# Kernel optimization log

Hardware: AMD Instinct MI355X
Metric: run time of the kernel (lower is better)

Reference implementation:

```python
import jax, jax.numpy as jnp
import numpy as np

B, N, C, H, D, K = 8, 2000, 64, 64, 16, 2  # batch, nodes, hidden, hidden_hidden, embed_dim, cheb_k


def setup_inputs() -> dict:
    key = jax.random.key(0)
    ks = jax.random.split(key, 12)
    f = lambda k, s, sc=1.0: jax.random.normal(k, s, dtype=jnp.float32) * sc
    return {
        "z": f(ks[0], (B, N, C)),
        "W_in": f(ks[1], (H, C), 0.1),
        "b_in": f(ks[2], (H,), 0.1),
        "W_out": f(ks[3], (C * C, H), 0.05),
        "b_out": f(ks[4], (C * C,), 0.05),
        "emb": f(ks[5], (N, D), 0.1),
        "wp": f(ks[6], (D, K, H, H), 0.1),
        "bp": f(ks[7], (D, H), 0.1),
        "w1": f(ks[8], (C,)),
        "w2": f(ks[9], (C,)),
        "vs": f(ks[10], (N, N), 0.02),
        "bs": f(ks[11], (N, N), 0.02),
    }


def reference(z, W_in, b_in, W_out, b_out, emb, wp, bp, w1, w2, vs, bs):
    # linear_in + relu: (B,N,C) -> (B,N,H)
    h = jax.nn.relu(jnp.einsum("bnc,hc->bnh", z, W_in) + b_in)

    # data-adaptive graph: softmax over rows of relu(emb @ emb^T)
    A = jax.nn.softmax(jax.nn.relu(emb @ emb.T), axis=1)  # (N,N)
    S = jnp.stack([jnp.eye(N, dtype=z.dtype), A], axis=0)  # (K,N,N), cheb_k=2

    # spatial attention on h (x = h.unsqueeze(1), f_in == H == C)
    e1 = h @ w1  # (B,N)
    e2 = h @ w2  # (B,N)
    prod = e1[:, :, None] * e2[:, None, :]  # (B,N,N) outer product
    E = jax.nn.softmax(
        jnp.einsum("nm,bmp->bnp", vs, jax.nn.sigmoid(prod + bs)), axis=-1
    )  # (B,N,N)

    # batched supports: E.unsqueeze(1) @ S -> (B,K,N,N)
    sup = jnp.einsum("bnm,kmp->bknp", E, S)

    # node-adaptive weights / bias
    weights = jnp.einsum("nd,dkio->nkio", emb, wp)  # (N,K,H,H)
    bias = emb @ bp  # (N,H)

    # graph conv
    x_g = jnp.einsum("bknm,bmc->bnkc", sup, h)  # (B,N,K,H)
    g = jnp.einsum("bnki,nkio->bno", x_g, weights) + bias  # (B,N,H)

    # linear_out + view + tanh, scaled by 0.1
    out = jnp.tanh(jnp.einsum("bnh,oh->bno", g, W_out) + b_out)
    return 0.1 * out.reshape(B, N, C, C)
```

## Files before the change

kernel.cpp:

```cpp
#include <hip/hip_runtime.h>
#include <hip/hip_bf16.h>

#define NN 2000
#define NP 2048
#define BB 8
#define HH 64
#define DD 16

typedef __hip_bfloat16 bf16;
typedef short bf16x8 __attribute__((ext_vector_type(8)));
typedef float f32x4 __attribute__((ext_vector_type(4)));

__device__ __forceinline__ float fast_sigmoid(float x) {
    return 1.0f / (1.0f + __expf(-x));
}
__device__ __forceinline__ float fast_tanh(float x) {
    float e = __expf(2.0f * x);
    return 1.0f - 2.0f / (e + 1.0f);
}

__device__ __forceinline__ void glds16(const void* g, void* l) {
    __builtin_amdgcn_global_load_lds(
        (const __attribute__((address_space(1))) void*)g,
        (__attribute__((address_space(3))) void*)l, 16, 0, 0);
}

__global__ __launch_bounds__(256) void k_h(
        const float* __restrict__ z, const float* __restrict__ W_in,
        const float* __restrict__ b_in, const float* __restrict__ w1,
        const float* __restrict__ w2, float* __restrict__ h,
        float* __restrict__ e1, float* __restrict__ e2) {
    __shared__ float WT[64 * 65];
    __shared__ float zs[4][64];
    int t = threadIdx.x;
    int lane = t & 63, ty = t >> 6;
    int bn0 = blockIdx.x * 4;
    for (int i = t; i < 64 * 64; i += 256) {
        int hh = i >> 6, c = i & 63;
        WT[c * 65 + hh] = W_in[i];
    }
    zs[ty][lane] = z[(size_t)(bn0 + ty) * 64 + lane];
    __syncthreads();
    float acc = b_in[lane];
    #pragma unroll
    for (int c = 0; c < 64; c++) acc += zs[ty][c] * WT[c * 65 + lane];
    float hv = fmaxf(acc, 0.0f);
    h[(size_t)(bn0 + ty) * 64 + lane] = hv;
    float p1 = hv * w1[lane], p2 = hv * w2[lane];
    #pragma unroll
    for (int off = 32; off > 0; off >>= 1) {
        p1 += __shfl_down(p1, off);
        p2 += __shfl_down(p2, off);
    }
    if (lane == 0) { e1[bn0 + ty] = p1; e2[bn0 + ty] = p2; }
}

__global__ __launch_bounds__(256) void k_A(const float* __restrict__ emb,
                                           bf16* __restrict__ A) {
    int i = blockIdx.x, t = threadIdx.x;
    if (i >= NN) {
        for (int j = t; j < NP; j += 256) A[(size_t)i * NP + j] = __float2bfloat16(0.0f);
        return;
    }
    __shared__ float ei[DD];
    __shared__ float rowbuf[NP];
    __shared__ float red[256];
    if (t < DD) ei[t] = emb[i * DD + t];
    __syncthreads();
    float lmax = -1e30f;
    for (int j = t; j < NP; j += 256) {
        float s = 0.0f;
        if (j < NN) {
            #pragma unroll
            for (int d = 0; d < DD; d++) s += ei[d] * emb[j * DD + d];
            s = fmaxf(s, 0.0f);
            lmax = fmaxf(lmax, s);
        }
        rowbuf[j] = s;
    }
    red[t] = lmax; __syncthreads();
    for (int o = 128; o > 0; o >>= 1) { if (t < o) red[t] = fmaxf(red[t], red[t + o]); __syncthreads(); }
    float mx = red[0];
    __syncthreads();
    float lsum = 0.0f;
    for (int j = t; j < NN; j += 256) {
        float e = __expf(rowbuf[j] - mx);
        rowbuf[j] = e; lsum += e;
    }
    red[t] = lsum; __syncthreads();
    for (int o = 128; o > 0; o >>= 1) { if (t < o) red[t] += red[t + o]; __syncthreads(); }
    float inv = 1.0f / red[0];
    for (int j = t; j < NP; j += 256)
        A[(size_t)i * NP + j] = __float2bfloat16(j < NN ? rowbuf[j] * inv : 0.0f);
}

__global__ __launch_bounds__(256) void k_misc(
        const float* __restrict__ vs, bf16* __restrict__ vs_bf,
        const float* __restrict__ W_out, bf16* __restrict__ Wo_bf,
        const float* __restrict__ emb, const float* __restrict__ wp,
        float* __restrict__ Wn_all) {
    __shared__ float embs[128 * 16];
    int bid = blockIdx.x, t = threadIdx.x;
    if (bid < 16384) {
        int id = bid * 256 + t;
        int n = id >> 11, m = id & (NP - 1);
        float v = (n < NN && m < NN) ? vs[n * NN + m] : 0.0f;
        vs_bf[id] = __float2bfloat16(v);
        return;
    }
    if (bid < 16384 + 1024) {
        int id = (bid - 16384) * 256 + t;
        Wo_bf[id] = __float2bfloat16(W_out[id]);
        return;
    }
    int wb = bid - 17408;
    int n0 = (wb & 15) * 128;
    int jo = (wb >> 4) * 256 + t;
    float wv[16];
    #pragma unroll
    for (int d = 0; d < 16; d++) wv[d] = wp[(size_t)d * 8192 + jo];
    for (int s = t; s < 128 * 16; s += 256) {
        int i = s >> 4, d = s & 15;
        int n = n0 + i;
        embs[s] = (n < NN) ? emb[n * 16 + d] : 0.f;
    }
    __syncthreads();
    for (int i = 0; i < 128; i++) {
        int n = n0 + i;
        if (n >= NN) break;
        const f32x4* ev = (const f32x4*)&embs[i * 16];
        f32x4 e0 = ev[0], e1 = ev[1], e2 = ev[2], e3 = ev[3];
        float a = 0.f;
        #pragma unroll
        for (int q = 0; q < 4; q++) a += e0[q] * wv[q];
        #pragma unroll
        for (int q = 0; q < 4; q++) a += e1[q] * wv[4 + q];
        #pragma unroll
        for (int q = 0; q < 4; q++) a += e2[q] * wv[8 + q];
        #pragma unroll
        for (int q = 0; q < 4; q++) a += e3[q] * wv[12 + q];
        Wn_all[(size_t)n * 8192 + jo] = a;
    }
}

__global__ __launch_bounds__(256) void k_hT(const float* __restrict__ h,
                                            bf16* __restrict__ hTcat,
                                            bf16* __restrict__ hsT) {
    __shared__ float tile[64 * 65];
    int nt = blockIdx.x, b = blockIdx.y;
    int tx = threadIdx.x & 63, ty = threadIdx.x >> 6;
    int n0 = nt * 64;
    for (int i = ty * 16; i < ty * 16 + 16; i++) {
        int n = n0 + i;
        tile[i * 65 + tx] = (n < NN) ? h[((size_t)b * NN + n) * 64 + tx] : 0.0f;
    }
    __syncthreads();
    for (int i = ty * 16; i < ty * 16 + 16; i++) {
        bf16 v = __float2bfloat16(tile[tx * 65 + i]);
        hTcat[((size_t)b * 64 + i) * NP + n0 + tx] = v;
        hsT[((size_t)b * 128 + i) * NP + n0 + tx] = v;
    }
}

__global__ __launch_bounds__(256) void k_redT(const float* __restrict__ AhPart,
                                              bf16* __restrict__ hsT) {
    __shared__ float tile[64 * 65];
    int pt = blockIdx.x, b = blockIdx.y;
    int tx = threadIdx.x & 63, ty = threadIdx.x >> 6;
    int p0 = pt * 64, q0 = b * 64;
    const long long TOT = (long long)NP * 512;
    for (int i = ty * 16; i < ty * 16 + 16; i++) {
        long long base = ((long long)p0 + i) * 512 + q0 + tx;
        float s = AhPart[base];
        #pragma unroll
        for (int sl = 1; sl < 4; sl++) s += AhPart[sl * TOT + base];
        tile[i * 65 + tx] = s;
    }
    __syncthreads();
    for (int i = ty * 16; i < ty * 16 + 16; i++)
        hsT[((size_t)b * 128 + 64 + i) * NP + p0 + tx] =
            __float2bfloat16(tile[tx * 65 + i]);
}

__global__ __launch_bounds__(256) void k_Tt(const float* __restrict__ e1,
                                            const float* __restrict__ e2,
                                            const float* __restrict__ bs,
                                            bf16* __restrict__ Tt) {
    __shared__ float tile[64 * 65];
    int b = blockIdx.z;
    e1 += (size_t)b * NN;
    e2 += (size_t)b * NN;
    Tt += (size_t)b * NP * NP;
    int mt = blockIdx.x, pt = blockIdx.y;
    int tx = threadIdx.x & 63, ty = threadIdx.x >> 6;
    int m0 = mt * 64, p0 = pt * 64;
    int p = p0 + tx;
    float e2v = (p < NN) ? e2[p] : 0.0f;
    for (int i = ty * 16; i < ty * 16 + 16; i++) {
        int m = m0 + i;
        float v = 0.0f;
        if (m < NN && p < NN)
            v = fast_sigmoid(e1[m] * e2v + bs[(size_t)m * NN + p]);
        tile[i * 65 + tx] = v;
    }
    __syncthreads();
    for (int i = ty * 16; i < ty * 16 + 16; i++)
        Tt[((size_t)p0 + i) * NP + m0 + tx] = __float2bfloat16(tile[tx * 65 + i]);
}

__global__ __launch_bounds__(512, 4) void k_gemm256pv(
        const bf16* __restrict__ X, const bf16* __restrict__ Yt,
        const bf16* __restrict__ hsT, float* __restrict__ xgPart,
        float* __restrict__ rsPart,
        int K, int ldx, int ldy, long long sY, long long sHs) {
    __shared__ short LDSb[32768];
    short* Asb = LDSb;
    short* Bsb = LDSb + 8192;
    int bx = blockIdx.x, by = blockIdx.y, z = blockIdx.z;
    const bf16* Xp = X;
    const bf16* Yp = Yt + (long long)z * sY;
    int tid = threadIdx.x;
    int m0 = bx * 128, n0 = by * 256;
    int wave = tid >> 6, lane = tid & 63;
    int wr = wave >> 2, wc = wave & 3;
    int fr = lane & 15, kq = lane >> 4;

    f32x4 zero = {0.f, 0.f, 0.f, 0.f};
    f32x4 acc[4][4];
    #pragma unroll
    for (int i = 0; i < 4; i++)
        #pragma unroll
        for (int j = 0; j < 4; j++) acc[i][j] = zero;

    int r4 = tid >> 2, slot = tid & 3;
    int scol = (slot ^ ((r4 >> 1) & 3)) * 8;
    const bf16* xsrc = Xp + (long long)(m0 + r4) * ldx + scol;
    const bf16* ysrc = Yp + (long long)(n0 + r4) * ldy + scol;
    short* Ad = Asb + tid * 8;
    short* Bd = Bsb + tid * 8;

    auto STAGE = [&](int tile) {
        int bufA = (tile & 1) * 4096;
        int bufB = (tile & 1) * 8192;
        long long ko = (long long)tile * 32;
        glds16(xsrc + ko, Ad + bufA);
        glds16(ysrc + ko, Bd + bufB);
        glds16(ysrc + 128 * (long long)ldy + ko, Bd + bufB + 4096);
    };

    int aoff[4], boff[4];
    #pragma unroll
    for (int i = 0; i < 4; i++) {
        int row = wr * 64 + i * 16 + fr;
        aoff[i] = row * 32 + ((kq ^ ((row >> 1) & 3)) << 3);
    }
    #pragma unroll
    for (int j = 0; j < 4; j++) {
        int row = wc * 64 + j * 16 + fr;
        boff[j] = row * 32 + ((kq ^ ((row >> 1) & 3)) << 3);
    }

    int NT = K >> 5;
    STAGE(0); STAGE(1);
    asm volatile("s_waitcnt vmcnt(3)" ::: "memory");
    __builtin_amdgcn_s_barrier();

    for (int t = 0; t < NT; t++) {
        const short* Ab = Asb + (t & 1) * 4096;
        const short* Bb = Bsb + (t & 1) * 8192;
        bf16x8 a[4], b[4];
        #pragma unroll
        for (int i = 0; i < 4; i++) a[i] = *(const bf16x8*)(Ab + aoff[i]);
        #pragma unroll
        for (int j = 0; j < 4; j++) b[j] = *(const bf16x8*)(Bb + boff[j]);
        __builtin_amdgcn_s_setprio(1);
        #pragma unroll
        for (int i = 0; i < 4; i++)
            #pragma unroll
            for (int j = 0; j < 4; j++)
                acc[i][j] = __builtin_amdgcn_mfma_f32_16x16x32_bf16(a[i], b[j], acc[i][j], 0, 0, 0);
        __builtin_amdgcn_s_setprio(0);
        __builtin_amdgcn_sched_barrier(0);
        __builtin_amdgcn_s_barrier();
        __builtin_amdgcn_sched_barrier(0);
        if (t + 2 < NT) {
            STAGE(t + 2);
            asm volatile("s_waitcnt vmcnt(3)" ::: "memory");
        } else if (t + 1 < NT) {
            asm volatile("s_waitcnt vmcnt(0)" ::: "memory");
        }
        __builtin_amdgcn_s_barrier();
    }
    __syncthreads();

    int rq = kq * 4;
    #pragma unroll
    for (int i = 0; i < 4; i++) {
        #pragma unroll
        for (int r = 0; r < 4; r++) {
            int lrow = wr * 64 + i * 16 + rq + r;
            float rs = 0.f;
            #pragma unroll
            for (int j = 0; j < 4; j++) {
                int lcol = wc * 64 + j * 16 + fr;
                float e = (n0 + lcol < NN) ? __expf(acc[i][j][r]) : 0.f;
                bf16 bv = __float2bfloat16(e);
                int sl = (lcol >> 3) ^ (lrow & 7);
                LDSb[lrow * 256 + sl * 8 + (lcol & 7)] = *(short*)&bv;
                rs += e;
            }
            rs += __shfl_xor(rs, 1);
            rs += __shfl_xor(rs, 2);
            rs += __shfl_xor(rs, 4);
            rs += __shfl_xor(rs, 8);
            if (fr == 0)
                rsPart[((long long)z * 32 + by * 4 + wc) * NP + m0 + lrow] = rs;
        }
    }
    __syncthreads();

    const bf16* hz = hsT + (long long)z * sHs;
    int wr2 = wave >> 2, wc2 = wave & 3;
    f32x4 acc2[4][2];
    #pragma unroll
    for (int i = 0; i < 4; i++)
        #pragma unroll
        for (int jj = 0; jj < 2; jj++) acc2[i][jj] = zero;
    #pragma unroll
    for (int ks = 0; ks < 8; ks++) {
        bf16x8 a2[4], b2[2];
        #pragma unroll
        for (int i = 0; i < 4; i++) {
            int row = wr2 * 64 + i * 16 + fr;
            int sl = (ks * 4 + kq) ^ (row & 7);
            a2[i] = *(const bf16x8*)(LDSb + row * 256 + sl * 8);
        }
        #pragma unroll
        for (int jj = 0; jj < 2; jj++)
            b2[jj] = *(const bf16x8*)(hz + (long long)(wc2 * 32 + jj * 16 + fr) * NP
                                      + n0 + ks * 32 + kq * 8);
        #pragma unroll
        for (int i = 0; i < 4; i++)
            #pragma unroll
            for (int jj = 0; jj < 2; jj++)
                acc2[i][jj] = __builtin_amdgcn_mfma_f32_16x16x32_bf16(a2[i], b2[jj], acc2[i][jj], 0, 0, 0);
    }
    #pragma unroll
    for (int i = 0; i < 4; i++)
        #pragma unroll
        for (int jj = 0; jj < 2; jj++) {
            int jcol = wc2 * 32 + jj * 16 + fr;
            #pragma unroll
            for (int r = 0; r < 4; r++) {
                int n = m0 + wr2 * 64 + i * 16 + rq + r;
                xgPart[(long long)n * 8192 + by * 1024 + z * 128 + jcol] = acc2[i][jj][r];
            }
        }
}

template<bool TANH, int KSPLIT>
__global__ __launch_bounds__(256) void k_gemm_bt(
        const bf16* __restrict__ X, const bf16* __restrict__ Yt,
        float* __restrict__ C, const float* __restrict__ bias,
        int K, int ldx, int ldy, int ldc,
        long long sX, long long sY, long long sC, long long sSlice) {
    __shared__ short As[128 * 32];
    __shared__ short Bs[128 * 32];
    int zz = blockIdx.z;
    int ks = 0;
    if (KSPLIT > 1) { ks = zz % KSPLIT; zz /= KSPLIT; }
    const bf16* Xp = X + (long long)zz * sX;
    const bf16* Yp = Yt + (long long)zz * sY;
    float* Cp = C + (long long)zz * sC + (long long)ks * sSlice;
    int tid = threadIdx.x;
    int m0 = blockIdx.x * 128, n0 = blockIdx.y * 128;
    int wave = tid >> 6, lane = tid & 63;
    int wm = (wave >> 1) * 64, wn = (wave & 1) * 64;
    int fr = lane & 15, kq = lane >> 4;

    f32x4 zero = {0.f, 0.f, 0.f, 0.f};
    f32x4 acc[4][4];
    #pragma unroll
    for (int i = 0; i < 4; i++)
        #pragma unroll
        for (int j = 0; j < 4; j++) acc[i][j] = zero;

    int lrow = lane >> 2, lcol = (lane & 3) * 8;
    const bf16* xg0 = Xp + (long long)(m0 + wave * 16 + lrow) * ldx + lcol;
    const bf16* xg1 = xg0 + (long long)64 * ldx;
    const bf16* yg0 = Yp + (long long)(n0 + wave * 16 + lrow) * ldy + lcol;
    const bf16* yg1 = yg0 + (long long)64 * ldy;
    short* lA0 = As + wave * 512;
    short* lA1 = As + (wave + 4) * 512;
    short* lB0 = Bs + wave * 512;
    short* lB1 = Bs + (wave + 4) * 512;

    int kbeg = (KSPLIT > 1) ? ks * (K / KSPLIT) : 0;
    int kend = kbeg + K / KSPLIT;
    for (int k0 = kbeg; k0 < kend; k0 += 32) {
        __syncthreads();
        glds16(xg0 + k0, lA0);
        glds16(xg1 + k0, lA1);
        glds16(yg0 + k0, lB0);
        glds16(yg1 + k0, lB1);
        __syncthreads();
        bf16x8 a[4], b[4];
        #pragma unroll
        for (int i = 0; i < 4; i++)
            a[i] = *(const bf16x8*)(As + (wm + i * 16 + fr) * 32 + kq * 8);
        #pragma unroll
        for (int j = 0; j < 4; j++)
            b[j] = *(const bf16x8*)(Bs + (wn + j * 16 + fr) * 32 + kq * 8);
        #pragma unroll
        for (int i = 0; i < 4; i++)
            #pragma unroll
            for (int j = 0; j < 4; j++)
                acc[i][j] = __builtin_amdgcn_mfma_f32_16x16x32_bf16(a[i], b[j], acc[i][j], 0, 0, 0);
    }
    int rq = kq * 4;
    for (int i = 0; i < 4; i++)
        for (int j = 0; j < 4; j++) {
            int col = n0 + wn + j * 16 + fr;
            float bv = TANH ? bias[col] : 0.0f;
            #pragma unroll
            for (int r = 0; r < 4; r++) {
                int row = m0 + wm + i * 16 + rq + r;
                float v = acc[i][j][r];
                Cp[(long long)row * ldc + col] =
                    TANH ? 0.1f * fast_tanh(v + bv) : v;
            }
        }
}

__global__ __launch_bounds__(256) void k_g(
        const float* __restrict__ Wn_all, const float* __restrict__ bp,
        const float* __restrict__ emb, const float* __restrict__ xgPart,
        const float* __restrict__ rsPart, bf16* __restrict__ gbf) {
    __shared__ float Wn[8192];
    __shared__ float xgc[8192];
    __shared__ float xgs[1024];
    __shared__ float biass[64];
    __shared__ float invs[8];
    int n = blockIdx.x, t = threadIdx.x;
    if (t < 8) {
        float s = 0.f;
        #pragma unroll
        for (int y = 0; y < 32; y++)
            s += rsPart[((size_t)t * 32 + y) * NP + n];
        invs[t] = 1.0f / s;
    }
    if (t >= 64 && t < 128) {
        int o = t - 64;
        float a = 0.f;
        #pragma unroll
        for (int d = 0; d < 16; d++) a += emb[n * 16 + d] * bp[d * 64 + o];
        biass[o] = a;
    }
    {
        const f32x4* src = (const f32x4*)(Wn_all + (size_t)n * 8192);
        const f32x4* xsrc = (const f32x4*)(xgPart + (size_t)n * 8192);
        f32x4* dst = (f32x4*)Wn;
        f32x4* xdst = (f32x4*)xgc;
        #pragma unroll
        for (int s = 0; s < 8; s++) {
            dst[s * 256 + t] = src[s * 256 + t];
            xdst[s * 256 + t] = xsrc[s * 256 + t];
        }
    }
    __syncthreads();
    for (int s = 0; s < 4; s++) {
        int id = t + s * 256;
        int b = id >> 7, j = id & 127;
        float a = xgc[b * 128 + j];
        #pragma unroll
        for (int by = 1; by < 8; by++) a += xgc[by * 1024 + b * 128 + j];
        xgs[id] = a * invs[b];
    }
    __syncthreads();
    int o = t & 63, bh = t >> 6;
    for (int half = 0; half < 2; half++) {
        int b = bh + half * 4;
        float a = biass[o];
        for (int j = 0; j < 128; j++) a += xgs[b * 128 + j] * Wn[j * 64 + o];
        gbf[((size_t)b * NN + n) * 64 + o] = __float2bfloat16(a);
    }
}

extern "C" void kernel_launch(void* const* d_in, const int* in_sizes, int n_in,
                              void* d_out, int out_size, void* d_ws, size_t ws_size,
                              hipStream_t stream) {
    const float* z     = (const float*)d_in[0];
    const float* W_in  = (const float*)d_in[1];
    const float* b_in  = (const float*)d_in[2];
    const float* W_out = (const float*)d_in[3];
    const float* b_out = (const float*)d_in[4];
    const float* emb   = (const float*)d_in[5];
    const float* wp    = (const float*)d_in[6];
    const float* bp    = (const float*)d_in[7];
    const float* w1    = (const float*)d_in[8];
    const float* w2    = (const float*)d_in[9];
    const float* vs    = (const float*)d_in[10];
    const float* bs    = (const float*)d_in[11];

    char* p = (char*)d_ws;
    auto alloc = [&](size_t bytes) -> char* {
        char* r = p;
        p += (bytes + 255) & ~(size_t)255;
        return r;
    };
    float* h       = (float*)alloc((size_t)BB * NN * 64 * 4);
    float* e1      = (float*)alloc((size_t)BB * NN * 4);
    float* e2      = (float*)alloc((size_t)BB * NN * 4);
    bf16*  A_bf    = (bf16*) alloc((size_t)NP * NP * 2);
    bf16*  vs_bf   = (bf16*) alloc((size_t)NP * NP * 2);
    bf16*  Tt_all  = (bf16*) alloc((size_t)BB * NP * NP * 2);
    float* rsPart  = (float*)alloc((size_t)BB * 32 * NP * 4);
    bf16*  hTcat   = (bf16*) alloc((size_t)512 * NP * 2);
    float* AhPart  = (float*)alloc((size_t)4 * NP * 512 * 4);
    bf16*  hsT     = (bf16*) alloc((size_t)BB * 128 * NP * 2);
    float* xgPart  = (float*)alloc((size_t)NP * 8192 * 4);
    bf16*  gbf     = (bf16*) alloc((size_t)BB * NN * 64 * 2);
    bf16*  Wo_bf   = (bf16*) alloc((size_t)4096 * 64 * 2);
    float* Wn_all  = (float*)alloc((size_t)NN * 8192 * 4);

    k_h<<<BB * NN / 4, 256, 0, stream>>>(z, W_in, b_in, w1, w2, h, e1, e2);
    k_A<<<NP, 256, 0, stream>>>(emb, A_bf);
    k_misc<<<16384 + 1024 + 512, 256, 0, stream>>>(vs, vs_bf, W_out, Wo_bf,
                                                   emb, wp, Wn_all);
    k_hT<<<dim3(NP / 64, BB), 256, 0, stream>>>(h, hTcat, hsT);

    k_gemm_bt<false, 4><<<dim3(16, 4, 4), 256, 0, stream>>>(
        A_bf, hTcat, AhPart, nullptr, NP, NP, NP, 512,
        0, 0, 0, (long long)NP * 512);
    k_redT<<<dim3(NP / 64, BB), 256, 0, stream>>>(AhPart, hsT);

    k_Tt<<<dim3(NP / 64, NP / 64, BB), 256, 0, stream>>>(e1, e2, bs, Tt_all);
    k_gemm256pv<<<dim3(16, 8, BB), 512, 0, stream>>>(
        vs_bf, Tt_all, hsT, xgPart, rsPart, NP, NP, NP,
        (long long)NP * NP, (long long)128 * NP);

    k_g<<<NN, 256, 0, stream>>>(Wn_all, bp, emb, xgPart, rsPart, gbf);
    k_gemm_bt<true, 1><<<dim3(125, 32, 1), 256, 0, stream>>>(
        gbf, Wo_bf, (float*)d_out, b_out, 64, 64, 64, 4096, 0, 0, 0, 0);
}
```

Before: 658.4 us.

## Merge preprocessing kernels into one mega-kernel and stream xgPart in k_g

Five independent preprocessing kernels (Tt sigmoid transpose, vs conversion, softmax adjacency, node weights, h transpose, W_out conversion) are folded into a single launch that dispatches on block index. This removes several launch gaps and lets small, underfilled phases overlap with the large elementwise ones. k_g also drops its 32KB shared staging of xgPart and reads partials straight from global memory, with the row-sum reduction staged through shared memory, so LDS use falls and occupancy can rise. The cost is one large kernel whose shared-memory size is set by the biggest branch and whose phases have very different block durations.

```diff
diff --git a/kernel.cpp b/kernel.cpp
--- a/kernel.cpp
+++ b/kernel.cpp
@@ -55,52 +55,43 @@
     if (lane == 0) { e1[bn0 + ty] = p1; e2[bn0 + ty] = p2; }
 }
 
-__global__ __launch_bounds__(256) void k_A(const float* __restrict__ emb,
-                                           bf16* __restrict__ A) {
-    int i = blockIdx.x, t = threadIdx.x;
-    if (i >= NN) {
-        for (int j = t; j < NP; j += 256) A[(size_t)i * NP + j] = __float2bfloat16(0.0f);
+__global__ __launch_bounds__(256) void k_mega(
+        const float* __restrict__ e1, const float* __restrict__ e2,
+        const float* __restrict__ bs, bf16* __restrict__ Tt,
+        const float* __restrict__ vs, bf16* __restrict__ vs_bf,
+        const float* __restrict__ emb, bf16* __restrict__ A,
+        const float* __restrict__ wp, float* __restrict__ Wn_all,
+        const float* __restrict__ h, bf16* __restrict__ hTcat,
+        bf16* __restrict__ hsT,
+        const float* __restrict__ W_out, bf16* __restrict__ Wo_bf) {
+    __shared__ float smem[4160];
+    int bid = blockIdx.x, t = threadIdx.x;
+
+    if (bid < 8192) {
+        int b = bid >> 10, rem = bid & 1023;
+        int mt = rem & 31, pt = rem >> 5;
+        const float* e1b = e1 + (size_t)b * NN;
+        const float* e2b = e2 + (size_t)b * NN;
+        bf16* Tb = Tt + (size_t)b * NP * NP;
+        float* tile = smem;
+        int tx = t & 63, ty = t >> 6;
+        int m0 = mt * 64, p0 = pt * 64;
+        int p = p0 + tx;
+        float e2v = (p < NN) ? e2b[p] : 0.0f;
+        for (int i = ty * 16; i < ty * 16 + 16; i++) {
+            int m = m0 + i;
+            float v = 0.0f;
+            if (m < NN && p < NN)
+                v = fast_sigmoid(e1b[m] * e2v + bs[(size_t)m * NN + p]);
+            tile[i * 65 + tx] = v;
+        }
+        __syncthreads();
+        for (int i = ty * 16; i < ty * 16 + 16; i++)
+            Tb[((size_t)p0 + i) * NP + m0 + tx] =
+                __float2bfloat16(tile[tx * 65 + i]);
         return;
     }
-    __shared__ float ei[DD];
-    __shared__ float rowbuf[NP];
-    __shared__ float red[256];
-    if (t < DD) ei[t] = emb[i * DD + t];
-    __syncthreads();
-    float lmax = -1e30f;
-    for (int j = t; j < NP; j += 256) {
-        float s = 0.0f;
-        if (j < NN) {
-            #pragma unroll
-            for (int d = 0; d < DD; d++) s += ei[d] * emb[j * DD + d];
-            s = fmaxf(s, 0.0f);
-            lmax = fmaxf(lmax, s);
-        }
-        rowbuf[j] = s;
-    }
-    red[t] = lmax; __syncthreads();
-    for (int o = 128; o > 0; o >>= 1) { if (t < o) red[t] = fmaxf(red[t], red[t + o]); __syncthreads(); }
-    float mx = red[0];
-    __syncthreads();
-    float lsum = 0.0f;
-    for (int j = t; j < NN; j += 256) {
-        float e = __expf(rowbuf[j] - mx);
-        rowbuf[j] = e; lsum += e;
-    }
-    red[t] = lsum; __syncthreads();
-    for (int o = 128; o > 0; o >>= 1) { if (t < o) red[t] += red[t + o]; __syncthreads(); }
-    float inv = 1.0f / red[0];
-    for (int j = t; j < NP; j += 256)
-        A[(size_t)i * NP + j] = __float2bfloat16(j < NN ? rowbuf[j] * inv : 0.0f);
-}
-
-__global__ __launch_bounds__(256) void k_misc(
-        const float* __restrict__ vs, bf16* __restrict__ vs_bf,
-        const float* __restrict__ W_out, bf16* __restrict__ Wo_bf,
-        const float* __restrict__ emb, const float* __restrict__ wp,
-        float* __restrict__ Wn_all) {
-    __shared__ float embs[128 * 16];
-    int bid = blockIdx.x, t = threadIdx.x;
+    bid -= 8192;
     if (bid < 16384) {
         int id = bid * 256 + t;
         int n = id >> 11, m = id & (NP - 1);
@@ -108,57 +99,99 @@
         vs_bf[id] = __float2bfloat16(v);
         return;
     }
-    if (bid < 16384 + 1024) {
-        int id = (bid - 16384) * 256 + t;
+    bid -= 16384;
+    if (bid < 2048) {
+        int i = bid;
+        if (i >= NN) {
+            for (int j = t; j < NP; j += 256) A[(size_t)i * NP + j] = __float2bfloat16(0.0f);
+            return;
+        }
+        float* rowbuf = smem;
+        float* red = smem + 2048;
+        float* ei = smem + 2304;
+        if (t < DD) ei[t] = emb[i * DD + t];
+        __syncthreads();
+        float lmax = -1e30f;
+        for (int j = t; j < NP; j += 256) {
+            float s = 0.0f;
+            if (j < NN) {
+                #pragma unroll
+                for (int d = 0; d < DD; d++) s += ei[d] * emb[j * DD + d];
+                s = fmaxf(s, 0.0f);
+                lmax = fmaxf(lmax, s);
+            }
+            rowbuf[j] = s;
+        }
+        red[t] = lmax; __syncthreads();
+        for (int o = 128; o > 0; o >>= 1) { if (t < o) red[t] = fmaxf(red[t], red[t + o]); __syncthreads(); }
+        float mx = red[0];
+        __syncthreads();
+        float lsum = 0.0f;
+        for (int j = t; j < NN; j += 256) {
+            float e = __expf(rowbuf[j] - mx);
+            rowbuf[j] = e; lsum += e;
+        }
+        red[t] = lsum; __syncthreads();
+        for (int o = 128; o > 0; o >>= 1) { if (t < o) red[t] += red[t + o]; __syncthreads(); }
+        float inv = 1.0f / red[0];
+        for (int j = t; j < NP; j += 256)
+            A[(size_t)i * NP + j] = __float2bfloat16(j < NN ? rowbuf[j] * inv : 0.0f);
+        return;
+    }
+    bid -= 2048;
+    if (bid < 512) {
+        float* embs = smem;
+        int n0 = (bid & 15) * 128;
+        int jo = (bid >> 4) * 256 + t;
+        float wv[16];
+        #pragma unroll
+        for (int d = 0; d < 16; d++) wv[d] = wp[(size_t)d * 8192 + jo];
+        for (int s = t; s < 128 * 16; s += 256) {
+            int i = s >> 4, d = s & 15;
+            int n = n0 + i;
+            embs[s] = (n < NN) ? emb[n * 16 + d] : 0.f;
+        }
+        __syncthreads();
+        for (int i = 0; i < 128; i++) {
+            int n = n0 + i;
+            if (n >= NN) break;
+            const f32x4* ev = (const f32x4*)&embs[i * 16];
+            f32x4 ea = ev[0], eb = ev[1], ec = ev[2], ed = ev[3];
+            float a = 0.f;
+            #pragma unroll
+            for (int q = 0; q < 4; q++) a += ea[q] * wv[q];
+            #pragma unroll
+            for (int q = 0; q < 4; q++) a += eb[q] * wv[4 + q];
+            #pragma unroll
+            for (int q = 0; q < 4; q++) a += ec[q] * wv[8 + q];
+            #pragma unroll
+            for (int q = 0; q < 4; q++) a += ed[q] * wv[12 + q];
+            Wn_all[(size_t)n * 8192 + jo] = a;
+        }
+        return;
+    }
+    bid -= 512;
+    if (bid < 256) {
+        float* tile = smem;
+        int nt = bid & 31, b = bid >> 5;
+        int tx = t & 63, ty = t >> 6;
+        int n0 = nt * 64;
+        for (int i = ty * 16; i < ty * 16 + 16; i++) {
+            int n = n0 + i;
+            tile[i * 65 + tx] = (n < NN) ? h[((size_t)b * NN + n) * 64 + tx] : 0.0f;
+        }
+        __syncthreads();
+        for (int i = ty * 16; i < ty * 16 + 16; i++) {
+            bf16 v = __float2bfloat16(tile[tx * 65 + i]);
+            hTcat[((size_t)b * 64 + i) * NP + n0 + tx] = v;
+            hsT[((size_t)b * 128 + i) * NP + n0 + tx] = v;
+        }
+        return;
+    }
+    bid -= 256;
+    {
+        int id = bid * 256 + t;
         Wo_bf[id] = __float2bfloat16(W_out[id]);
-        return;
-    }
-    int wb = bid - 17408;
-    int n0 = (wb & 15) * 128;
-    int jo = (wb >> 4) * 256 + t;
-    float wv[16];
-    #pragma unroll
-    for (int d = 0; d < 16; d++) wv[d] = wp[(size_t)d * 8192 + jo];
-    for (int s = t; s < 128 * 16; s += 256) {
-        int i = s >> 4, d = s & 15;
-        int n = n0 + i;
-        embs[s] = (n < NN) ? emb[n * 16 + d] : 0.f;
-    }
-    __syncthreads();
-    for (int i = 0; i < 128; i++) {
-        int n = n0 + i;
-        if (n >= NN) break;
-        const f32x4* ev = (const f32x4*)&embs[i * 16];
-        f32x4 e0 = ev[0], e1 = ev[1], e2 = ev[2], e3 = ev[3];
-        float a = 0.f;
-        #pragma unroll
-        for (int q = 0; q < 4; q++) a += e0[q] * wv[q];
-        #pragma unroll
-        for (int q = 0; q < 4; q++) a += e1[q] * wv[4 + q];
-        #pragma unroll
-        for (int q = 0; q < 4; q++) a += e2[q] * wv[8 + q];
-        #pragma unroll
-        for (int q = 0; q < 4; q++) a += e3[q] * wv[12 + q];
-        Wn_all[(size_t)n * 8192 + jo] = a;
-    }
-}
-
-__global__ __launch_bounds__(256) void k_hT(const float* __restrict__ h,
-                                            bf16* __restrict__ hTcat,
-                                            bf16* __restrict__ hsT) {
-    __shared__ float tile[64 * 65];
-    int nt = blockIdx.x, b = blockIdx.y;
-    int tx = threadIdx.x & 63, ty = threadIdx.x >> 6;
-    int n0 = nt * 64;
-    for (int i = ty * 16; i < ty * 16 + 16; i++) {
-        int n = n0 + i;
-        tile[i * 65 + tx] = (n < NN) ? h[((size_t)b * NN + n) * 64 + tx] : 0.0f;
-    }
-    __syncthreads();
-    for (int i = ty * 16; i < ty * 16 + 16; i++) {
-        bf16 v = __float2bfloat16(tile[tx * 65 + i]);
-        hTcat[((size_t)b * 64 + i) * NP + n0 + tx] = v;
-        hsT[((size_t)b * 128 + i) * NP + n0 + tx] = v;
     }
 }
 
@@ -180,32 +213,6 @@
     for (int i = ty * 16; i < ty * 16 + 16; i++)
         hsT[((size_t)b * 128 + 64 + i) * NP + p0 + tx] =
             __float2bfloat16(tile[tx * 65 + i]);
-}
-
-__global__ __launch_bounds__(256) void k_Tt(const float* __restrict__ e1,
-                                            const float* __restrict__ e2,
-                                            const float* __restrict__ bs,
-                                            bf16* __restrict__ Tt) {
-    __shared__ float tile[64 * 65];
-    int b = blockIdx.z;
-    e1 += (size_t)b * NN;
-    e2 += (size_t)b * NN;
-    Tt += (size_t)b * NP * NP;
-    int mt = blockIdx.x, pt = blockIdx.y;
-    int tx = threadIdx.x & 63, ty = threadIdx.x >> 6;
-    int m0 = mt * 64, p0 = pt * 64;
-    int p = p0 + tx;
-    float e2v = (p < NN) ? e2[p] : 0.0f;
-    for (int i = ty * 16; i < ty * 16 + 16; i++) {
-        int m = m0 + i;
-        float v = 0.0f;
-        if (m < NN && p < NN)
-            v = fast_sigmoid(e1[m] * e2v + bs[(size_t)m * NN + p]);
-        tile[i * 65 + tx] = v;
-    }
-    __syncthreads();
-    for (int i = ty * 16; i < ty * 16 + 16; i++)
-        Tt[((size_t)p0 + i) * NP + m0 + tx] = __float2bfloat16(tile[tx * 65 + i]);
 }
 
 __global__ __launch_bounds__(512, 4) void k_gemm256pv(
@@ -437,18 +444,12 @@
         const float* __restrict__ emb, const float* __restrict__ xgPart,
         const float* __restrict__ rsPart, bf16* __restrict__ gbf) {
     __shared__ float Wn[8192];
-    __shared__ float xgc[8192];
     __shared__ float xgs[1024];
     __shared__ float biass[64];
     __shared__ float invs[8];
+    __shared__ float rsred[256];
     int n = blockIdx.x, t = threadIdx.x;
-    if (t < 8) {
-        float s = 0.f;
-        #pragma unroll
-        for (int y = 0; y < 32; y++)
-            s += rsPart[((size_t)t * 32 + y) * NP + n];
-        invs[t] = 1.0f / s;
-    }
+    rsred[t] = rsPart[(size_t)t * NP + n];
     if (t >= 64 && t < 128) {
         int o = t - 64;
         float a = 0.f;
@@ -458,22 +459,25 @@
     }
     {
         const f32x4* src = (const f32x4*)(Wn_all + (size_t)n * 8192);
-        const f32x4* xsrc = (const f32x4*)(xgPart + (size_t)n * 8192);
         f32x4* dst = (f32x4*)Wn;
-        f32x4* xdst = (f32x4*)xgc;
-        #pragma unroll
-        for (int s = 0; s < 8; s++) {
-            dst[s * 256 + t] = src[s * 256 + t];
-            xdst[s * 256 + t] = xsrc[s * 256 + t];
-        }
+        #pragma unroll
+        for (int s = 0; s < 8; s++) dst[s * 256 + t] = src[s * 256 + t];
+    }
+    __syncthreads();
+    if (t < 8) {
+        float s = 0.f;
+        #pragma unroll
+        for (int y = 0; y < 32; y++) s += rsred[t * 32 + y];
+        invs[t] = 1.0f / s;
     }
     __syncthreads();
     for (int s = 0; s < 4; s++) {
         int id = t + s * 256;
         int b = id >> 7, j = id & 127;
-        float a = xgc[b * 128 + j];
-        #pragma unroll
-        for (int by = 1; by < 8; by++) a += xgc[by * 1024 + b * 128 + j];
+        const float* xp = xgPart + (size_t)n * 8192 + b * 128 + j;
+        float a = xp[0];
+        #pragma unroll
+        for (int by = 1; by < 8; by++) a += xp[by * 1024];
         xgs[id] = a * invs[b];
     }
     __syncthreads();
@@ -524,17 +528,16 @@
     float* Wn_all  = (float*)alloc((size_t)NN * 8192 * 4);
 
     k_h<<<BB * NN / 4, 256, 0, stream>>>(z, W_in, b_in, w1, w2, h, e1, e2);
-    k_A<<<NP, 256, 0, stream>>>(emb, A_bf);
-    k_misc<<<16384 + 1024 + 512, 256, 0, stream>>>(vs, vs_bf, W_out, Wo_bf,
-                                                   emb, wp, Wn_all);
-    k_hT<<<dim3(NP / 64, BB), 256, 0, stream>>>(h, hTcat, hsT);
+
+    k_mega<<<8192 + 16384 + 2048 + 512 + 256 + 1024, 256, 0, stream>>>(
+        e1, e2, bs, Tt_all, vs, vs_bf, emb, A_bf, wp, Wn_all,
+        h, hTcat, hsT, W_out, Wo_bf);
 
     k_gemm_bt<false, 4><<<dim3(16, 4, 4), 256, 0, stream>>>(
         A_bf, hTcat, AhPart, nullptr, NP, NP, NP, 512,
         0, 0, 0, (long long)NP * 512);
     k_redT<<<dim3(NP / 64, BB), 256, 0, stream>>>(AhPart, hsT);
 
-    k_Tt<<<dim3(NP / 64, NP / 64, BB), 256, 0, stream>>>(e1, e2, bs, Tt_all);
     k_gemm256pv<<<dim3(16, 8, BB), 512, 0, stream>>>(
         vs_bf, Tt_all, hsT, xgPart, rsPart, NP, NP, NP,
         (long long)NP * NP, (long long)128 * NP);
```

Result: faster. 620.3 us (-5.8%).
